# Kernel optimization log

Hardware: AMD Instinct MI355X
Metric: run time of the kernel (lower is better)

## Reference

```python
import jax, jax.numpy as jnp
import numpy as np

N = 100000
E = 1600000
D = 128

def _degrees(idx, n):
    d = jax.ops.segment_sum(jnp.ones(idx.shape[0], jnp.float32), idx, num_segments=n)
    return jnp.clip(d, 1.0)

def _gconv(feat, src, dst, W, b, residual, act):
    n = feat.shape[0]
    norm_out = _degrees(src, n) ** -0.5            # [N] out-degree norm
    h = feat * norm_out[:, None]                   # scale src features
    msgs = h[src]                                  # gather [E, D]
    agg = jax.ops.segment_sum(msgs, dst, num_segments=n)  # scatter-sum [N, D]
    rst = agg @ W.T + b                            # dense linear
    norm_in = _degrees(dst, n) ** -0.5             # [N] in-degree norm
    rst = rst * norm_in[:, None]
    if residual:
        rst = rst + feat                           # identity residual (in==out)
    if act:
        rst = jax.nn.relu(rst)
    return rst

def setup_inputs() -> dict:
    key = jax.random.key(0)
    ks = jax.random.split(key, 10)
    feat = jax.random.normal(ks[0], (N, D), jnp.float32)
    src = jax.random.randint(ks[1], (E,), 0, N)
    dst = jax.random.randint(ks[2], (E,), 0, N)
    s = 1.0 / np.sqrt(D)
    W1 = jax.random.uniform(ks[3], (D, D), jnp.float32, -s, s)
    b1 = jax.random.uniform(ks[4], (D,), jnp.float32, -s, s)
    W2 = jax.random.uniform(ks[5], (D, D), jnp.float32, -s, s)
    b2 = jax.random.uniform(ks[6], (D,), jnp.float32, -s, s)
    W3 = jax.random.uniform(ks[7], (D, D), jnp.float32, -s, s)
    b3 = jax.random.uniform(ks[8], (D,), jnp.float32, -s, s)
    return {"feat": feat, "src": src, "dst": dst,
            "W1": W1, "b1": b1, "W2": W2, "b2": b2, "W3": W3, "b3": b3}

def reference(feat, src, dst, W1, b1, W2, b2, W3, b3):
    # 3-layer GCN, dropout=0, norm=None, encoding=False:
    # layers 0,1: residual + relu; layer 2: no residual, no activation
    h = _gconv(feat, src, dst, W1, b1, residual=True, act=True)
    h = _gconv(h, src, dst, W2, b2, residual=True, act=True)
    h = _gconv(h, src, dst, W3, b3, residual=False, act=False)
    return h
```

## Files before the change

kernel.cpp:

```cpp
#include <hip/hip_runtime.h>

#define NN 100000
#define EE 1600000
#define DD 128
#define NB 512
#define CAP 4608
#define CHUNK 8192

typedef __attribute__((ext_vector_type(8))) short short8v;
typedef __attribute__((ext_vector_type(4))) float f32x4;
typedef __attribute__((ext_vector_type(8))) unsigned short ushort8v;

static __device__ __forceinline__ unsigned short f2bf(float x) {
  unsigned u = __builtin_bit_cast(unsigned, x);
  return (unsigned short)((u + 0x7FFFu + ((u >> 16) & 1u)) >> 16);
}
static __device__ __forceinline__ float bf2f(unsigned short u) {
  return __builtin_bit_cast(float, (unsigned)u << 16);
}

__global__ __launch_bounds__(512) void initcur_k(int* __restrict__ cur_d,
                                                 int* __restrict__ cur_s) {
  int t = threadIdx.x;
  cur_d[t] = t * CAP;
  cur_s[t] = t * CAP;
}

__global__ __launch_bounds__(256) void split_k(const int* __restrict__ src,
                                               const int* __restrict__ dst,
                                               int* __restrict__ cur_d,
                                               int* __restrict__ cur_s,
                                               unsigned* __restrict__ tmp_d,
                                               unsigned char* __restrict__ tmp_s) {
  __shared__ int hd[NB], hs[NB], bd[NB], bs[NB];
  int t = threadIdx.x;
  int base = blockIdx.x * CHUNK;
  int end = base + CHUNK < EE ? base + CHUNK : EE;
  for (int b = t; b < NB; b += 256) { hd[b] = 0; hs[b] = 0; }
  __syncthreads();
  for (int i = base + t; i < end; i += 256) {
    atomicAdd(&hd[dst[i] >> 8], 1);
    atomicAdd(&hs[src[i] >> 8], 1);
  }
  __syncthreads();
  for (int b = t; b < NB; b += 256) {
    bd[b] = hd[b] ? atomicAdd(&cur_d[b], hd[b]) : 0;
    bs[b] = hs[b] ? atomicAdd(&cur_s[b], hs[b]) : 0;
    hd[b] = 0;
    hs[b] = 0;
  }
  __syncthreads();
  for (int i = base + t; i < end; i += 256) {
    int s = src[i];
    int d = dst[i];
    int bin = d >> 8;
    int r = atomicAdd(&hd[bin], 1);
    int pos = bd[bin] + r;
    if (pos < (bin + 1) * CAP) tmp_d[pos] = ((unsigned)(d & 255) << 17) | (unsigned)s;
    bin = s >> 8;
    r = atomicAdd(&hs[bin], 1);
    pos = bs[bin] + r;
    if (pos < (bin + 1) * CAP) tmp_s[pos] = (unsigned char)(s & 255);
  }
}

__global__ __launch_bounds__(512) void scan512_k(const int* __restrict__ cur_d,
                                                 int* __restrict__ dstart) {
  __shared__ int lds[512];
  int t = threadIdx.x;
  int v = cur_d[t] - t * CAP;
  v = v < CAP ? v : CAP;
  lds[t] = v;
  __syncthreads();
  int run = v;
  for (int off = 1; off < 512; off <<= 1) {
    int y = (t >= off) ? lds[t - off] : 0;
    __syncthreads();
    run += y;
    lds[t] = run;
    __syncthreads();
  }
  dstart[t] = run - v;
}

__global__ __launch_bounds__(256) void bucket_dst_k(const unsigned* __restrict__ tmp_d,
                                                    const int* __restrict__ cur_d,
                                                    const int* __restrict__ dstart,
                                                    int* __restrict__ csr,
                                                    int* __restrict__ row_s,
                                                    int* __restrict__ row_e,
                                                    float* __restrict__ norm_in) {
  __shared__ unsigned stage[CAP];
  __shared__ int h[256], sc[256], rk[256];
  int b = blockIdx.x;
  int t = threadIdx.x;
  int cnt = cur_d[b] - b * CAP;
  cnt = cnt < CAP ? cnt : CAP;
  int ds = dstart[b];
  for (int i = t; i < cnt; i += 256) stage[i] = tmp_d[b * CAP + i];
  h[t] = 0;
  __syncthreads();
  for (int i = t; i < cnt; i += 256) atomicAdd(&h[stage[i] >> 17], 1);
  __syncthreads();
  int v = h[t];
  sc[t] = v;
  __syncthreads();
  int run = v;
  for (int off = 1; off < 256; off <<= 1) {
    int y = (t >= off) ? sc[t - off] : 0;
    __syncthreads();
    run += y;
    sc[t] = run;
    __syncthreads();
  }
  int excl = run - v;
  int n = b * 256 + t;
  if (n < NN) {
    row_s[n] = ds + excl;
    row_e[n] = ds + excl + v;
    norm_in[n] = rsqrtf((float)(v > 1 ? v : 1));
  }
  rk[t] = excl;
  __syncthreads();
  for (int i = t; i < cnt; i += 256) {
    unsigned w = stage[i];
    int r = atomicAdd(&rk[w >> 17], 1);
    csr[ds + r] = (int)(w & 0x1FFFFu);
  }
}

__global__ __launch_bounds__(256) void bucket_src_k(const unsigned char* __restrict__ tmp_s,
                                                    const int* __restrict__ cur_s,
                                                    float* __restrict__ norm_out) {
  __shared__ int h[256];
  int b = blockIdx.x;
  int t = threadIdx.x;
  int cnt = cur_s[b] - b * CAP;
  cnt = cnt < CAP ? cnt : CAP;
  h[t] = 0;
  __syncthreads();
  const unsigned char* p = tmp_s + b * CAP;
  for (int i = t; i < cnt; i += 256) atomicAdd(&h[p[i]], 1);
  __syncthreads();
  int n = b * 256 + t;
  if (n < NN) norm_out[n] = rsqrtf((float)(h[t] > 1 ? h[t] : 1));
}

__global__ __launch_bounds__(256) void wconv_k(const float* __restrict__ w,
                                               unsigned short* __restrict__ o) {
  int i = blockIdx.x * 256 + threadIdx.x;
  float4 v = *reinterpret_cast<const float4*>(w + i * 4);
  unsigned short r0 = f2bf(v.x), r1 = f2bf(v.y), r2 = f2bf(v.z), r3 = f2bf(v.w);
  ushort4 pk = make_ushort4(r0, r1, r2, r3);
  *reinterpret_cast<ushort4*>(o + i * 4) = pk;
}

__global__ __launch_bounds__(256) void hconv_k(const float* __restrict__ feat,
                                               const float* __restrict__ no,
                                               unsigned short* __restrict__ h) {
  int i = blockIdx.x * 256 + threadIdx.x;
  int node = i >> 4;
  int lane = i & 15;
  float n = no[node];
  const float* p = feat + node * DD + lane * 8;
  float4 a = *reinterpret_cast<const float4*>(p);
  float4 b = *reinterpret_cast<const float4*>(p + 4);
  ushort8v o;
  o[0] = f2bf(a.x * n); o[1] = f2bf(a.y * n); o[2] = f2bf(a.z * n); o[3] = f2bf(a.w * n);
  o[4] = f2bf(b.x * n); o[5] = f2bf(b.y * n); o[6] = f2bf(b.z * n); o[7] = f2bf(b.w * n);
  *reinterpret_cast<ushort8v*>(h + node * DD + lane * 8) = o;
}

__global__ __launch_bounds__(256) void aggregate_k(const unsigned short* __restrict__ h,
                                                   const int* __restrict__ csr,
                                                   const int* __restrict__ row_s,
                                                   const int* __restrict__ row_e,
                                                   unsigned short* __restrict__ aggout) {
  int node = (blockIdx.x * 256 + threadIdx.x) >> 4;
  int lane = threadIdx.x & 15;
  int e0 = row_s[node];
  int e1 = row_e[node];
  float acc[8] = {0.f, 0.f, 0.f, 0.f, 0.f, 0.f, 0.f, 0.f};
  int e = e0;
  for (; e + 2 <= e1; e += 2) {
    int s0 = csr[e];
    int s1 = csr[e + 1];
    ushort8v u = *reinterpret_cast<const ushort8v*>(h + (size_t)s0 * DD + lane * 8);
    ushort8v v = *reinterpret_cast<const ushort8v*>(h + (size_t)s1 * DD + lane * 8);
#pragma unroll
    for (int i = 0; i < 8; ++i) acc[i] += bf2f(u[i]) + bf2f(v[i]);
  }
  if (e < e1) {
    int s0 = csr[e];
    ushort8v u = *reinterpret_cast<const ushort8v*>(h + (size_t)s0 * DD + lane * 8);
#pragma unroll
    for (int i = 0; i < 8; ++i) acc[i] += bf2f(u[i]);
  }
  ushort8v o;
#pragma unroll
  for (int i = 0; i < 8; ++i) o[i] = f2bf(acc[i]);
  *reinterpret_cast<ushort8v*>(aggout + (size_t)node * DD + lane * 8) = o;
}

__global__ __launch_bounds__(256) void gemm_k(const unsigned short* __restrict__ A,
                                              const unsigned short* __restrict__ Wb,
                                              const float* __restrict__ bias,
                                              const float* __restrict__ nin,
                                              const float* __restrict__ nout,
                                              const float* __restrict__ resid,
                                              float* __restrict__ outp,
                                              unsigned short* __restrict__ hnext,
                                              int mode) {
  int wid = threadIdx.x >> 6;
  int lane = threadIdx.x & 63;
  int rbase = blockIdx.x * 64 + wid * 16;
  int l15 = lane & 15;
  int kgrp = lane >> 4;

  int arow = rbase + l15;
  int arow_c = arow < NN ? arow : NN - 1;
  const unsigned short* ap = A + (size_t)arow_c * DD + kgrp * 8;
  short8v af0 = *reinterpret_cast<const short8v*>(ap);
  short8v af1 = *reinterpret_cast<const short8v*>(ap + 32);
  short8v af2 = *reinterpret_cast<const short8v*>(ap + 64);
  short8v af3 = *reinterpret_cast<const short8v*>(ap + 96);

  int nd0 = rbase + kgrp * 4;
  float nin4[4], nout4[4];
#pragma unroll
  for (int r = 0; r < 4; ++r) {
    int n = nd0 + r;
    int nc = n < NN ? n : NN - 1;
    nin4[r] = nin[nc];
    nout4[r] = (mode ? nout[nc] : 0.f);
  }

  for (int ct = 0; ct < 8; ++ct) {
    const unsigned short* wp = Wb + (size_t)(ct * 16 + l15) * DD + kgrp * 8;
    short8v b0 = *reinterpret_cast<const short8v*>(wp);
    short8v b1 = *reinterpret_cast<const short8v*>(wp + 32);
    short8v b2 = *reinterpret_cast<const short8v*>(wp + 64);
    short8v b3 = *reinterpret_cast<const short8v*>(wp + 96);
    f32x4 acc = {0.f, 0.f, 0.f, 0.f};
    acc = __builtin_amdgcn_mfma_f32_16x16x32_bf16(af0, b0, acc, 0, 0, 0);
    acc = __builtin_amdgcn_mfma_f32_16x16x32_bf16(af1, b1, acc, 0, 0, 0);
    acc = __builtin_amdgcn_mfma_f32_16x16x32_bf16(af2, b2, acc, 0, 0, 0);
    acc = __builtin_amdgcn_mfma_f32_16x16x32_bf16(af3, b3, acc, 0, 0, 0);

    int col = ct * 16 + l15;
    float bj = bias[col];
#pragma unroll
    for (int r = 0; r < 4; ++r) {
      int node = nd0 + r;
      if (node < NN) {
        float v = (acc[r] + bj) * nin4[r];
        size_t idx = (size_t)node * DD + col;
        if (mode) {
          v += resid[idx];
          v = fmaxf(v, 0.f);
          outp[idx] = v;
          hnext[idx] = f2bf(v * nout4[r]);
        } else {
          outp[idx] = v;
        }
      }
    }
  }
}

extern "C" void kernel_launch(void* const* d_in, const int* in_sizes, int n_in,
                              void* d_out, int out_size, void* d_ws, size_t ws_size,
                              hipStream_t stream) {
  const float* feat = (const float*)d_in[0];
  const int* src = (const int*)d_in[1];
  const int* dst = (const int*)d_in[2];
  const float* W1 = (const float*)d_in[3];
  const float* b1 = (const float*)d_in[4];
  const float* W2 = (const float*)d_in[5];
  const float* b2 = (const float*)d_in[6];
  const float* W3 = (const float*)d_in[7];
  const float* b3 = (const float*)d_in[8];
  float* out = (float*)d_out;

  int* row_s = (int*)d_ws;
  int* row_e = row_s + NN;
  float* norm_out = (float*)(row_e + NN);
  float* norm_in = norm_out + NN;
  int* cur_d = (int*)(norm_in + NN);
  int* cur_s = cur_d + NB;
  int* dstart = cur_s + NB;
  int* pad = dstart + NB;
  unsigned short* Wbf = (unsigned short*)pad;
  int* csr = (int*)(Wbf + 3 * 16384);
  unsigned short* agg = (unsigned short*)(csr + EE);
  unsigned short* hbuf = agg + (size_t)NN * DD;

  unsigned* tmp_d = (unsigned*)d_out;
  unsigned char* tmp_s = (unsigned char*)d_out + (size_t)NB * CAP * 4;

  initcur_k<<<1, 512, 0, stream>>>(cur_d, cur_s);
  split_k<<<(EE + CHUNK - 1) / CHUNK, 256, 0, stream>>>(src, dst, cur_d, cur_s, tmp_d, tmp_s);
  scan512_k<<<1, 512, 0, stream>>>(cur_d, dstart);
  bucket_dst_k<<<NB, 256, 0, stream>>>(tmp_d, cur_d, dstart, csr, row_s, row_e, norm_in);
  bucket_src_k<<<NB, 256, 0, stream>>>(tmp_s, cur_s, norm_out);

  wconv_k<<<16, 256, 0, stream>>>(W1, Wbf);
  wconv_k<<<16, 256, 0, stream>>>(W2, Wbf + 16384);
  wconv_k<<<16, 256, 0, stream>>>(W3, Wbf + 32768);
  hconv_k<<<6250, 256, 0, stream>>>(feat, norm_out, hbuf);

  const int GG = (NN + 63) / 64;
  aggregate_k<<<6250, 256, 0, stream>>>(hbuf, csr, row_s, row_e, agg);
  gemm_k<<<GG, 256, 0, stream>>>(agg, Wbf, b1, norm_in, norm_out, feat, out, hbuf, 1);
  aggregate_k<<<6250, 256, 0, stream>>>(hbuf, csr, row_s, row_e, agg);
  gemm_k<<<GG, 256, 0, stream>>>(agg, Wbf + 16384, b2, norm_in, norm_out, out, out, hbuf, 1);
  aggregate_k<<<6250, 256, 0, stream>>>(hbuf, csr, row_s, row_e, agg);
  gemm_k<<<GG, 256, 0, stream>>>(agg, Wbf + 32768, b3, norm_in, norm_out, nullptr, out, nullptr, 0);
}
```

Baseline: 387.8 us.

## Fuse neighbor aggregation with MFMA linear layer into one per-layer kernel

Merges the gather-sum aggregation and the bf16 MFMA GEMM into a single kernel per layer. Each lane aggregates one node's 32-column slice directly into MFMA operand registers, so the agg buffer write/read round trip and one launch per layer disappear. The MFMA operands are swapped so each lane owns 4 contiguous output columns, which gives float4 epilogue stores. Ping-pong h buffers avoid read/write races. In exchange, each lane now serially walks a whole node's edge list (4x fewer threads per node), which cuts gather parallelism and raises register pressure.

```diff
diff --git a/kernel.cpp b/kernel.cpp
--- a/kernel.cpp
+++ b/kernel.cpp
@@ -150,8 +150,7 @@
                                                unsigned short* __restrict__ o) {
   int i = blockIdx.x * 256 + threadIdx.x;
   float4 v = *reinterpret_cast<const float4*>(w + i * 4);
-  unsigned short r0 = f2bf(v.x), r1 = f2bf(v.y), r2 = f2bf(v.z), r3 = f2bf(v.w);
-  ushort4 pk = make_ushort4(r0, r1, r2, r3);
+  ushort4 pk = make_ushort4(f2bf(v.x), f2bf(v.y), f2bf(v.z), f2bf(v.w));
   *reinterpret_cast<ushort4*>(o + i * 4) = pk;
 }
 
@@ -171,98 +170,112 @@
   *reinterpret_cast<ushort8v*>(h + node * DD + lane * 8) = o;
 }
 
-__global__ __launch_bounds__(256) void aggregate_k(const unsigned short* __restrict__ h,
-                                                   const int* __restrict__ csr,
-                                                   const int* __restrict__ row_s,
-                                                   const int* __restrict__ row_e,
-                                                   unsigned short* __restrict__ aggout) {
-  int node = (blockIdx.x * 256 + threadIdx.x) >> 4;
-  int lane = threadIdx.x & 15;
-  int e0 = row_s[node];
-  int e1 = row_e[node];
-  float acc[8] = {0.f, 0.f, 0.f, 0.f, 0.f, 0.f, 0.f, 0.f};
+__global__ __launch_bounds__(256) void layer_k(const unsigned short* __restrict__ h,
+                                               const int* __restrict__ csr,
+                                               const int* __restrict__ row_s,
+                                               const int* __restrict__ row_e,
+                                               const unsigned short* __restrict__ Wb,
+                                               const float* __restrict__ bias,
+                                               const float* __restrict__ nin,
+                                               const float* __restrict__ nout,
+                                               const float* __restrict__ resid,
+                                               float* __restrict__ outp,
+                                               unsigned short* __restrict__ hnext,
+                                               int mode) {
+  int wid = threadIdx.x >> 6;
+  int lane = threadIdx.x & 63;
+  int l15 = lane & 15;
+  int kgrp = lane >> 4;
+  int node = blockIdx.x * 64 + wid * 16 + l15;
+  int nodec = node < NN ? node : NN - 1;
+
+  int e0 = row_s[nodec];
+  int e1 = row_e[nodec];
+  float a0[8] = {0,0,0,0,0,0,0,0}, a1[8] = {0,0,0,0,0,0,0,0};
+  float a2[8] = {0,0,0,0,0,0,0,0}, a3[8] = {0,0,0,0,0,0,0,0};
+  const unsigned short* hb = h + kgrp * 8;
   int e = e0;
   for (; e + 2 <= e1; e += 2) {
     int s0 = csr[e];
     int s1 = csr[e + 1];
-    ushort8v u = *reinterpret_cast<const ushort8v*>(h + (size_t)s0 * DD + lane * 8);
-    ushort8v v = *reinterpret_cast<const ushort8v*>(h + (size_t)s1 * DD + lane * 8);
+    const unsigned short* p0 = hb + (size_t)s0 * DD;
+    const unsigned short* p1 = hb + (size_t)s1 * DD;
+    ushort8v u0 = *reinterpret_cast<const ushort8v*>(p0);
+    ushort8v u1 = *reinterpret_cast<const ushort8v*>(p0 + 32);
+    ushort8v u2 = *reinterpret_cast<const ushort8v*>(p0 + 64);
+    ushort8v u3 = *reinterpret_cast<const ushort8v*>(p0 + 96);
+    ushort8v v0 = *reinterpret_cast<const ushort8v*>(p1);
+    ushort8v v1 = *reinterpret_cast<const ushort8v*>(p1 + 32);
+    ushort8v v2 = *reinterpret_cast<const ushort8v*>(p1 + 64);
+    ushort8v v3 = *reinterpret_cast<const ushort8v*>(p1 + 96);
 #pragma unroll
-    for (int i = 0; i < 8; ++i) acc[i] += bf2f(u[i]) + bf2f(v[i]);
+    for (int i = 0; i < 8; ++i) {
+      a0[i] += bf2f(u0[i]) + bf2f(v0[i]);
+      a1[i] += bf2f(u1[i]) + bf2f(v1[i]);
+      a2[i] += bf2f(u2[i]) + bf2f(v2[i]);
+      a3[i] += bf2f(u3[i]) + bf2f(v3[i]);
+    }
   }
   if (e < e1) {
     int s0 = csr[e];
-    ushort8v u = *reinterpret_cast<const ushort8v*>(h + (size_t)s0 * DD + lane * 8);
+    const unsigned short* p0 = hb + (size_t)s0 * DD;
+    ushort8v u0 = *reinterpret_cast<const ushort8v*>(p0);
+    ushort8v u1 = *reinterpret_cast<const ushort8v*>(p0 + 32);
+    ushort8v u2 = *reinterpret_cast<const ushort8v*>(p0 + 64);
+    ushort8v u3 = *reinterpret_cast<const ushort8v*>(p0 + 96);
 #pragma unroll
-    for (int i = 0; i < 8; ++i) acc[i] += bf2f(u[i]);
-  }
-  ushort8v o;
+    for (int i = 0; i < 8; ++i) {
+      a0[i] += bf2f(u0[i]);
+      a1[i] += bf2f(u1[i]);
+      a2[i] += bf2f(u2[i]);
+      a3[i] += bf2f(u3[i]);
+    }
+  }
+  short8v b0, b1, b2, b3;
 #pragma unroll
-  for (int i = 0; i < 8; ++i) o[i] = f2bf(acc[i]);
-  *reinterpret_cast<ushort8v*>(aggout + (size_t)node * DD + lane * 8) = o;
-}
-
-__global__ __launch_bounds__(256) void gemm_k(const unsigned short* __restrict__ A,
-                                              const unsigned short* __restrict__ Wb,
-                                              const float* __restrict__ bias,
-                                              const float* __restrict__ nin,
-                                              const float* __restrict__ nout,
-                                              const float* __restrict__ resid,
-                                              float* __restrict__ outp,
-                                              unsigned short* __restrict__ hnext,
-                                              int mode) {
-  int wid = threadIdx.x >> 6;
-  int lane = threadIdx.x & 63;
-  int rbase = blockIdx.x * 64 + wid * 16;
-  int l15 = lane & 15;
-  int kgrp = lane >> 4;
-
-  int arow = rbase + l15;
-  int arow_c = arow < NN ? arow : NN - 1;
-  const unsigned short* ap = A + (size_t)arow_c * DD + kgrp * 8;
-  short8v af0 = *reinterpret_cast<const short8v*>(ap);
-  short8v af1 = *reinterpret_cast<const short8v*>(ap + 32);
-  short8v af2 = *reinterpret_cast<const short8v*>(ap + 64);
-  short8v af3 = *reinterpret_cast<const short8v*>(ap + 96);
-
-  int nd0 = rbase + kgrp * 4;
-  float nin4[4], nout4[4];
-#pragma unroll
-  for (int r = 0; r < 4; ++r) {
-    int n = nd0 + r;
-    int nc = n < NN ? n : NN - 1;
-    nin4[r] = nin[nc];
-    nout4[r] = (mode ? nout[nc] : 0.f);
-  }
+  for (int i = 0; i < 8; ++i) {
+    b0[i] = (short)f2bf(a0[i]);
+    b1[i] = (short)f2bf(a1[i]);
+    b2[i] = (short)f2bf(a2[i]);
+    b3[i] = (short)f2bf(a3[i]);
+  }
+
+  float ninv = nin[nodec];
+  float noutv = mode ? nout[nodec] : 0.f;
 
   for (int ct = 0; ct < 8; ++ct) {
     const unsigned short* wp = Wb + (size_t)(ct * 16 + l15) * DD + kgrp * 8;
-    short8v b0 = *reinterpret_cast<const short8v*>(wp);
-    short8v b1 = *reinterpret_cast<const short8v*>(wp + 32);
-    short8v b2 = *reinterpret_cast<const short8v*>(wp + 64);
-    short8v b3 = *reinterpret_cast<const short8v*>(wp + 96);
-    f32x4 acc = {0.f, 0.f, 0.f, 0.f};
-    acc = __builtin_amdgcn_mfma_f32_16x16x32_bf16(af0, b0, acc, 0, 0, 0);
-    acc = __builtin_amdgcn_mfma_f32_16x16x32_bf16(af1, b1, acc, 0, 0, 0);
-    acc = __builtin_amdgcn_mfma_f32_16x16x32_bf16(af2, b2, acc, 0, 0, 0);
-    acc = __builtin_amdgcn_mfma_f32_16x16x32_bf16(af3, b3, acc, 0, 0, 0);
-
-    int col = ct * 16 + l15;
-    float bj = bias[col];
-#pragma unroll
-    for (int r = 0; r < 4; ++r) {
-      int node = nd0 + r;
-      if (node < NN) {
-        float v = (acc[r] + bj) * nin4[r];
-        size_t idx = (size_t)node * DD + col;
-        if (mode) {
-          v += resid[idx];
-          v = fmaxf(v, 0.f);
-          outp[idx] = v;
-          hnext[idx] = f2bf(v * nout4[r]);
-        } else {
-          outp[idx] = v;
-        }
+    short8v w0 = *reinterpret_cast<const short8v*>(wp);
+    short8v w1 = *reinterpret_cast<const short8v*>(wp + 32);
+    short8v w2 = *reinterpret_cast<const short8v*>(wp + 64);
+    short8v w3 = *reinterpret_cast<const short8v*>(wp + 96);
+    f32x4 c = {0.f, 0.f, 0.f, 0.f};
+    c = __builtin_amdgcn_mfma_f32_16x16x32_bf16(w0, b0, c, 0, 0, 0);
+    c = __builtin_amdgcn_mfma_f32_16x16x32_bf16(w1, b1, c, 0, 0, 0);
+    c = __builtin_amdgcn_mfma_f32_16x16x32_bf16(w2, b2, c, 0, 0, 0);
+    c = __builtin_amdgcn_mfma_f32_16x16x32_bf16(w3, b3, c, 0, 0, 0);
+
+    if (node < NN) {
+      int j = ct * 16 + kgrp * 4;
+      float4 bj = *reinterpret_cast<const float4*>(bias + j);
+      size_t idx = (size_t)node * DD + j;
+      float4 v;
+      v.x = (c[0] + bj.x) * ninv;
+      v.y = (c[1] + bj.y) * ninv;
+      v.z = (c[2] + bj.z) * ninv;
+      v.w = (c[3] + bj.w) * ninv;
+      if (mode) {
+        float4 rs = *reinterpret_cast<const float4*>(resid + idx);
+        v.x = fmaxf(v.x + rs.x, 0.f);
+        v.y = fmaxf(v.y + rs.y, 0.f);
+        v.z = fmaxf(v.z + rs.z, 0.f);
+        v.w = fmaxf(v.w + rs.w, 0.f);
+        *reinterpret_cast<float4*>(outp + idx) = v;
+        ushort4 hn = make_ushort4(f2bf(v.x * noutv), f2bf(v.y * noutv),
+                                  f2bf(v.z * noutv), f2bf(v.w * noutv));
+        *reinterpret_cast<ushort4*>(hnext + idx) = hn;
+      } else {
+        *reinterpret_cast<float4*>(outp + idx) = v;
       }
     }
   }
@@ -292,8 +305,8 @@
   int* pad = dstart + NB;
   unsigned short* Wbf = (unsigned short*)pad;
   int* csr = (int*)(Wbf + 3 * 16384);
-  unsigned short* agg = (unsigned short*)(csr + EE);
-  unsigned short* hbuf = agg + (size_t)NN * DD;
+  unsigned short* hbuf = (unsigned short*)(csr + EE);
+  unsigned short* hbuf2 = hbuf + (size_t)NN * DD;
 
   unsigned* tmp_d = (unsigned*)d_out;
   unsigned char* tmp_s = (unsigned char*)d_out + (size_t)NB * CAP * 4;
@@ -309,11 +322,11 @@
   wconv_k<<<16, 256, 0, stream>>>(W3, Wbf + 32768);
   hconv_k<<<6250, 256, 0, stream>>>(feat, norm_out, hbuf);
 
-  const int GG = (NN + 63) / 64;
-  aggregate_k<<<6250, 256, 0, stream>>>(hbuf, csr, row_s, row_e, agg);
-  gemm_k<<<GG, 256, 0, stream>>>(agg, Wbf, b1, norm_in, norm_out, feat, out, hbuf, 1);
-  aggregate_k<<<6250, 256, 0, stream>>>(hbuf, csr, row_s, row_e, agg);
-  gemm_k<<<GG, 256, 0, stream>>>(agg, Wbf + 16384, b2, norm_in, norm_out, out, out, hbuf, 1);
-  aggregate_k<<<6250, 256, 0, stream>>>(hbuf, csr, row_s, row_e, agg);
-  gemm_k<<<GG, 256, 0, stream>>>(agg, Wbf + 32768, b3, norm_in, norm_out, nullptr, out, nullptr, 0);
-}
+  const int GB = (NN + 63) / 64;
+  layer_k<<<GB, 256, 0, stream>>>(hbuf, csr, row_s, row_e, Wbf, b1, norm_in,
+                                  norm_out, feat, out, hbuf2, 1);
+  layer_k<<<GB, 256, 0, stream>>>(hbuf2, csr, row_s, row_e, Wbf + 16384, b2, norm_in,
+                                  norm_out, out, out, hbuf, 1);
+  layer_k<<<GB, 256, 0, stream>>>(hbuf, csr, row_s, row_e, Wbf + 32768, b3, norm_in,
+                                  norm_out, nullptr, out, nullptr, 0);
+}
```

Result: no change. 389.1 us (+0.3%).
